# Kernel optimization log

Hardware: AMD Instinct MI355X
Metric: run time of the kernel (lower is better)

Reference implementation:

```python
import jax, jax.numpy as jnp
import numpy as np

EPS = 1e-5  # torch LayerNorm default
B, P, E, H = 16, 2048, 768, 256


def setup_inputs() -> dict:
    key = jax.random.key(0)
    k_x, k_qkv, k_lw = jax.random.split(key, 3)
    return {
        "x": jax.random.normal(k_x, (B, P, E), dtype=jnp.float32),
        "norm_w": jnp.ones((P, E), dtype=jnp.float32),
        "norm_b": jnp.zeros((P, E), dtype=jnp.float32),
        "qkv_w": jax.random.normal(k_qkv, (E, 3 * H), dtype=jnp.float32) * 0.02,
        "lin_w": jax.random.normal(k_lw, (E, H), dtype=jnp.float32) * 0.02,
        "lin_b": jnp.zeros((E,), dtype=jnp.float32),
    }


def reference(x, norm_w, norm_b, qkv_w, lin_w, lin_b):
    # LayerNorm over the last TWO dims (P, E) jointly, per batch element
    mean = jnp.mean(x, axis=(1, 2), keepdims=True)
    var = jnp.var(x, axis=(1, 2), keepdims=True)
    xn = (x - mean) * jax.lax.rsqrt(var + EPS) * norm_w + norm_b

    # QKV projection: [B,P,E] @ [E,3H] -> [B,P,3H]
    qkv = jnp.einsum("bpe,eh->bph", xn, qkv_w)
    q, k, v = jnp.split(qkv, 3, axis=2)  # each [B,P,H]

    # Unnormalized attention (no scale, no softmax)
    atten = jnp.einsum("bpd,bqd->bpq", q, k)  # [B,P,P]
    o = jnp.einsum("bpq,bqd->bpd", atten, v)  # [B,P,H]

    # Dropout p=0.0 (eval) -> identity; then Linear(H -> E) + ReLU
    out = jnp.einsum("bph,eh->bpe", o, lin_w) + lin_b
    return jax.nn.relu(out)
```

## Files before the change

kernel.cpp:

```cpp
#include <hip/hip_runtime.h>
#include <cstdio>
#include <cstdint>

typedef unsigned short u16;
typedef __bf16 bf16x8 __attribute__((ext_vector_type(8)));
typedef float floatx4 __attribute__((ext_vector_type(4)));

#define BB 16
#define PP 2048
#define EE 768
#define HH 256
#define PE (PP * EE)
#define MM (BB * PP)

__device__ __forceinline__ u16 f2bf(float f) {
  union { float f; uint32_t u; } v; v.f = f;
  return (u16)((v.u + 0x7fffu + ((v.u >> 16) & 1u)) >> 16);
}

__device__ __forceinline__ void gload16(const void* g, void* l) {
  typedef __attribute__((address_space(1))) const void GV;
  typedef __attribute__((address_space(3))) void LV;
  __builtin_amdgcn_global_load_lds((GV*)g, (LV*)l, 16, 0, 0);
}

__device__ __forceinline__ void zero_acc(floatx4 acc[4][4]) {
  const floatx4 z = {0.f, 0.f, 0.f, 0.f};
#pragma unroll
  for (int i = 0; i < 4; ++i)
#pragma unroll
    for (int j = 0; j < 4; ++j) acc[i][j] = z;
}

__device__ __forceinline__ void gemm_core(const u16* A, int lda, const u16* B, int ldb,
                                          int kIters, u16* As, u16* Bs,
                                          floatx4 acc[4][4]) {
  const int tid  = threadIdx.x;
  const int lane = tid & 63;
  const int wr   = (tid >> 7) & 1;
  const int wc   = (tid >> 6) & 1;
  const int srow = tid >> 3;
  const int scol = (tid & 7) << 3;
  const int mrow = lane & 15;
  const int kgrp = (lane >> 4) << 3;
  for (int kk = 0; kk < kIters; ++kk) {
    const u16* Ak = A + kk * 64;
    const u16* Bk = B + kk * 64;
    __syncthreads();
#pragma unroll
    for (int r = 0; r < 4; ++r) {
      gload16(Ak + (size_t)(r * 32 + srow) * lda + scol, (char*)As + r * 4096 + tid * 16);
      gload16(Bk + (size_t)(r * 32 + srow) * ldb + scol, (char*)Bs + r * 4096 + tid * 16);
    }
    __syncthreads();
#pragma unroll
    for (int kp = 0; kp < 2; ++kp) {
      const int ko = kp * 32 + kgrp;
      bf16x8 af[4], bq[4];
#pragma unroll
      for (int i = 0; i < 4; ++i) {
        af[i] = *(const bf16x8*)(As + (wr * 64 + i * 16 + mrow) * 64 + ko);
        bq[i] = *(const bf16x8*)(Bs + (wc * 64 + i * 16 + mrow) * 64 + ko);
      }
#pragma unroll
      for (int i = 0; i < 4; ++i)
#pragma unroll
        for (int j = 0; j < 4; ++j)
          acc[i][j] = __builtin_amdgcn_mfma_f32_16x16x32_bf16(af[i], bq[j], acc[i][j], 0, 0, 0);
    }
  }
}

template <typename F>
__device__ __forceinline__ void epilogue(floatx4 acc[4][4], F f) {
  const int lane = threadIdx.x & 63;
  const int wr = (threadIdx.x >> 7) & 1, wc = (threadIdx.x >> 6) & 1;
  const int r0 = (lane >> 4) * 4, c0 = lane & 15;
#pragma unroll
  for (int i = 0; i < 4; ++i)
#pragma unroll
    for (int j = 0; j < 4; ++j)
#pragma unroll
      for (int r = 0; r < 4; ++r)
        f(wr * 64 + i * 16 + r0 + r, wc * 64 + j * 16 + c0, acc[i][j][r]);
}

__global__ __launch_bounds__(256) void k_reduce1(const float* __restrict__ x,
                                                 float* __restrict__ psum,
                                                 float* __restrict__ psq) {
  const int b = blockIdx.y, blk = blockIdx.x, tid = threadIdx.x;
  const float4* xb = (const float4*)(x + (size_t)b * PE + (size_t)blk * 12288);
  float s = 0.f, q = 0.f;
#pragma unroll
  for (int i = 0; i < 12; ++i) {
    float4 v = xb[tid + i * 256];
    s += v.x + v.y + v.z + v.w;
    q += v.x * v.x + v.y * v.y + v.z * v.z + v.w * v.w;
  }
  for (int off = 32; off > 0; off >>= 1) { s += __shfl_down(s, off); q += __shfl_down(q, off); }
  __shared__ float ls[4], lq[4];
  if ((tid & 63) == 0) { ls[tid >> 6] = s; lq[tid >> 6] = q; }
  __syncthreads();
  if (tid == 0) {
    psum[b * 128 + blk] = ls[0] + ls[1] + ls[2] + ls[3];
    psq [b * 128 + blk] = lq[0] + lq[1] + lq[2] + lq[3];
  }
}

__global__ void k_reduce2(const float* __restrict__ psum, const float* __restrict__ psq,
                          float* __restrict__ stats) {
  const int b = blockIdx.x, tid = threadIdx.x;
  float s = psum[b * 128 + tid], q = psq[b * 128 + tid];
  for (int off = 32; off > 0; off >>= 1) { s += __shfl_down(s, off); q += __shfl_down(q, off); }
  __shared__ float ls[2], lq[2];
  if ((tid & 63) == 0) { ls[tid >> 6] = s; lq[tid >> 6] = q; }
  __syncthreads();
  if (tid == 0) {
    float S = ls[0] + ls[1], Q = lq[0] + lq[1];
    const float invN = 1.f / (float)PE;
    float mean = S * invN;
    float var = Q * invN - mean * mean;
    stats[b * 2] = mean;
    stats[b * 2 + 1] = rsqrtf(var + 1e-5f);
  }
}

__global__ __launch_bounds__(256) void k_ln(const float* __restrict__ x,
                                            const float* __restrict__ w,
                                            const float* __restrict__ bia,
                                            const float* __restrict__ stats,
                                            u16* __restrict__ xn) {
  const float4* x4 = (const float4*)x;
  const float4* w4 = (const float4*)w;
  const float4* b4 = (const float4*)bia;
  for (int vi = blockIdx.x * 256 + threadIdx.x; vi < (PE / 4) * BB; vi += gridDim.x * 256) {
    int bidx = vi / (PE / 4);
    int wi = vi - bidx * (PE / 4);
    float4 xv = x4[vi], wv = w4[wi], bv = b4[wi];
    float mean = stats[bidx * 2], rstd = stats[bidx * 2 + 1];
    ushort4 o;
    o.x = f2bf((xv.x - mean) * rstd * wv.x + bv.x);
    o.y = f2bf((xv.y - mean) * rstd * wv.y + bv.y);
    o.z = f2bf((xv.z - mean) * rstd * wv.z + bv.z);
    o.w = f2bf((xv.w - mean) * rstd * wv.w + bv.w);
    ((ushort4*)xn)[vi] = o;
  }
}

__global__ void k_transpose_w(const float* __restrict__ src, u16* __restrict__ dst) {
  __shared__ float t[32][33];
  const int e0 = blockIdx.x * 32, n0 = blockIdx.y * 32;
  const int tx = threadIdx.x, ty = threadIdx.y;
#pragma unroll
  for (int j = 0; j < 4; ++j)
    t[ty + j * 8][tx] = src[(size_t)(e0 + ty + j * 8) * 768 + n0 + tx];
  __syncthreads();
#pragma unroll
  for (int j = 0; j < 4; ++j)
    dst[(size_t)(n0 + ty + j * 8) * 768 + e0 + tx] = f2bf(t[tx][ty + j * 8]);
}

__global__ void k_cast(const float* __restrict__ src, u16* __restrict__ dst, int n4) {
  int i = blockIdx.x * 256 + threadIdx.x;
  if (i < n4) {
    float4 v = ((const float4*)src)[i];
    ushort4 o;
    o.x = f2bf(v.x); o.y = f2bf(v.y); o.z = f2bf(v.z); o.w = f2bf(v.w);
    ((ushort4*)dst)[i] = o;
  }
}

__global__ __launch_bounds__(256) void k_gemm_qkv(const u16* __restrict__ xn,
                                                  const u16* __restrict__ wT,
                                                  u16* __restrict__ qkv) {
  __shared__ __align__(16) u16 As[128 * 64], Bs[128 * 64];
  floatx4 acc[4][4];
  zero_acc(acc);
  const int tM = blockIdx.y * 128, tN = blockIdx.x * 128;
  gemm_core(xn + (size_t)tM * EE, EE, wT + (size_t)tN * EE, EE, 12, As, Bs, acc);
  epilogue(acc, [&](int gr, int gc, float v) {
    qkv[(size_t)(tM + gr) * EE + tN + gc] = f2bf(v);
  });
}

__global__ void k_transpose_kv(const u16* __restrict__ qkv, u16* __restrict__ kT,
                               u16* __restrict__ vT) {
  __shared__ u16 t[32][33];
  const int z = blockIdx.z, b = z >> 1, which = z & 1;
  const int p0 = blockIdx.x * 32, d0 = blockIdx.y * 32;
  const u16* src = qkv + (size_t)b * PE + HH + which * HH;
  u16* dst = (which ? vT : kT) + (size_t)b * (HH * PP);
  const int tx = threadIdx.x, ty = threadIdx.y;
#pragma unroll
  for (int j = 0; j < 4; ++j)
    t[ty + j * 8][tx] = src[(size_t)(p0 + ty + j * 8) * EE + d0 + tx];
  __syncthreads();
#pragma unroll
  for (int j = 0; j < 4; ++j)
    dst[(size_t)(d0 + ty + j * 8) * PP + p0 + tx] = t[tx][ty + j * 8];
}

__global__ __launch_bounds__(256) void k_gemm_wt(const u16* __restrict__ vT,
                                                 const u16* __restrict__ kT,
                                                 float* __restrict__ part) {
  __shared__ __align__(16) u16 As[128 * 64], Bs[128 * 64];
  floatx4 acc[4][4];
  zero_acc(acc);
  const int z = blockIdx.z, b = z >> 3, s = z & 7;
  const int tM = blockIdx.y * 128, tN = blockIdx.x * 128;
  const u16* A = vT + (size_t)b * (HH * PP) + (size_t)tM * PP + s * 256;
  const u16* B = kT + (size_t)b * (HH * PP) + (size_t)tN * PP + s * 256;
  gemm_core(A, PP, B, PP, 4, As, Bs, acc);
  float* P = part + (size_t)z * 65536;
  epilogue(acc, [&](int gr, int gc, float v) {
    P[(size_t)(tM + gr) * 256 + tN + gc] = v;
  });
}

__global__ void k_reduce_wt(const float* __restrict__ part, u16* __restrict__ Wt) {
  const int idx = blockIdx.x * 256 + threadIdx.x;
  const int b = idx >> 16, i = idx & 65535;
  const float* p = part + ((size_t)b << 19) + i;
  float s = 0.f;
#pragma unroll
  for (int t = 0; t < 8; ++t) s += p[(size_t)t << 16];
  Wt[idx] = f2bf(s);
}

__global__ __launch_bounds__(256) void k_gemm_o(const u16* __restrict__ qkv,
                                                const u16* __restrict__ Wt,
                                                u16* __restrict__ o) {
  __shared__ __align__(16) u16 As[128 * 64], Bs[128 * 64];
  floatx4 acc[4][4];
  zero_acc(acc);
  const int b = blockIdx.z;
  const int tM = blockIdx.y * 128, tN = blockIdx.x * 128;
  const u16* A = qkv + (size_t)b * PE + (size_t)tM * EE;
  const u16* B = Wt + (size_t)b * 65536 + (size_t)tN * 256;
  gemm_core(A, EE, B, 256, 4, As, Bs, acc);
  u16* ob = o + (size_t)b * (PP * HH);
  epilogue(acc, [&](int gr, int gc, float v) {
    ob[(size_t)(tM + gr) * HH + tN + gc] = f2bf(v);
  });
}

__global__ __launch_bounds__(256) void k_gemm_lin(const u16* __restrict__ o,
                                                  const u16* __restrict__ lw,
                                                  const float* __restrict__ lb,
                                                  float* __restrict__ out) {
  __shared__ __align__(16) u16 As[128 * 64], Bs[128 * 64];
  floatx4 acc[4][4];
  zero_acc(acc);
  const int tM = blockIdx.y * 128, tN = blockIdx.x * 128;
  gemm_core(o + (size_t)tM * HH, HH, lw + (size_t)tN * HH, HH, 4, As, Bs, acc);
  epilogue(acc, [&](int gr, int gc, float v) {
    out[(size_t)(tM + gr) * EE + tN + gc] = fmaxf(v + lb[tN + gc], 0.f);
  });
}

extern "C" void kernel_launch(void* const* d_in, const int* in_sizes, int n_in,
                              void* d_out, int out_size, void* d_ws, size_t ws_size,
                              hipStream_t stream) {
  (void)in_sizes; (void)n_in; (void)out_size;
  const float* x  = (const float*)d_in[0];
  const float* nw = (const float*)d_in[1];
  const float* nb = (const float*)d_in[2];
  const float* qw = (const float*)d_in[3];
  const float* lw = (const float*)d_in[4];
  const float* lb = (const float*)d_in[5];
  float* out = (float*)d_out;
  char* ws = (char*)d_ws;

  size_t off = 0;
  auto alloc = [&](size_t bytes) { size_t o = off; off += (bytes + 255) & ~(size_t)255; return o; };
  const size_t o_psum = alloc(16 * 128 * 4);
  const size_t o_psq  = alloc(16 * 128 * 4);
  const size_t o_st   = alloc(16 * 2 * 4);
  const size_t o_qwT  = alloc((size_t)768 * 768 * 2);
  const size_t o_lwB  = alloc((size_t)768 * 256 * 2);
  const size_t o_qkv  = alloc((size_t)MM * EE * 2);
  const size_t o_kT   = alloc((size_t)BB * HH * PP * 2);
  const size_t o_vT   = alloc((size_t)BB * HH * PP * 2);
  const size_t o_Wt   = alloc((size_t)BB * HH * HH * 2);
  const size_t need_base = off;
  const size_t region = (size_t)MM * EE * 2;

  char* big = (ws_size >= need_base + region) ? (ws + need_base) : (char*)d_out;
  static bool printed = false;
  if (!printed) {
    fprintf(stderr, "[vit] ws_size=%zu need=%zu big_in_out=%d\n",
            ws_size, need_base + region, big == (char*)d_out);
    printed = true;
  }

  float* psum = (float*)(ws + o_psum);
  float* psq  = (float*)(ws + o_psq);
  float* st   = (float*)(ws + o_st);
  u16* qwT    = (u16*)(ws + o_qwT);
  u16* lwB    = (u16*)(ws + o_lwB);
  u16* qkv    = (u16*)(ws + o_qkv);
  u16* kT     = (u16*)(ws + o_kT);
  u16* vT     = (u16*)(ws + o_vT);
  u16* Wt     = (u16*)(ws + o_Wt);
  u16* o_buf  = (u16*)(ws + o_kT);
  u16* xn     = (u16*)big;
  float* part = (float*)big;

  k_reduce1<<<dim3(128, 16), 256, 0, stream>>>(x, psum, psq);
  k_reduce2<<<16, 128, 0, stream>>>(psum, psq, st);
  k_ln<<<2048, 256, 0, stream>>>(x, nw, nb, st, xn);
  k_transpose_w<<<dim3(24, 24), dim3(32, 8), 0, stream>>>(qw, qwT);
  k_cast<<<192, 256, 0, stream>>>(lw, lwB, 768 * 256 / 4);
  k_gemm_qkv<<<dim3(6, 256), 256, 0, stream>>>(xn, qwT, qkv);
  k_transpose_kv<<<dim3(64, 8, 32), dim3(32, 8), 0, stream>>>(qkv, kT, vT);
  k_gemm_wt<<<dim3(2, 2, 128), 256, 0, stream>>>(vT, kT, part);
  k_reduce_wt<<<4096, 256, 0, stream>>>(part, Wt);
  k_gemm_o<<<dim3(2, 16, 16), 256, 0, stream>>>(qkv, Wt, o_buf);
  k_gemm_lin<<<dim3(6, 256), 256, 0, stream>>>(o_buf, lwB, lb, out);
}
```

Baseline: 354.6 us.

## Fold linear weight into per-batch KV product and fuse K/V transpose into QKV GEMM

Reassociates the chain so the per-batch K^T V matrix is multiplied by the linear weight first, giving a small per-batch 768x256 matrix. The output then comes from a single GEMM of Q against that matrix, removing the separate O GEMM and its intermediate buffer. The QKV GEMM epilogue now writes K and V already transposed through shared memory, which eliminates the standalone transpose kernel. All GEMMs use 1D grids with an XCD-aware block remap for cache locality. The extra bf16 rounding of the fused matrix can change numerical error slightly.

New measurement: 329.7 us. 1.08x faster.

```diff
diff --git a/kernel.cpp b/kernel.cpp
--- a/kernel.cpp
+++ b/kernel.cpp
@@ -1,5 +1,4 @@
 #include <hip/hip_runtime.h>
-#include <cstdio>
 #include <cstdint>
 
 typedef unsigned short u16;
@@ -22,6 +21,10 @@
   typedef __attribute__((address_space(1))) const void GV;
   typedef __attribute__((address_space(3))) void LV;
   __builtin_amdgcn_global_load_lds((GV*)g, (LV*)l, 16, 0, 0);
+}
+
+__device__ __forceinline__ int xcd_remap(int orig, int nwg) {
+  return (orig & 7) * (nwg >> 3) + (orig >> 3);
 }
 
 __device__ __forceinline__ void zero_acc(floatx4 acc[4][4]) {
@@ -172,44 +175,70 @@
 
 __global__ __launch_bounds__(256) void k_gemm_qkv(const u16* __restrict__ xn,
                                                   const u16* __restrict__ wT,
-                                                  u16* __restrict__ qkv) {
-  __shared__ __align__(16) u16 As[128 * 64], Bs[128 * 64];
+                                                  u16* __restrict__ q_buf,
+                                                  u16* __restrict__ kT,
+                                                  u16* __restrict__ vT) {
+  __shared__ __align__(16) u16 sbuf[128 * 64 * 2];
+  u16* As = sbuf;
+  u16* Bs = sbuf + 128 * 64;
   floatx4 acc[4][4];
   zero_acc(acc);
-  const int tM = blockIdx.y * 128, tN = blockIdx.x * 128;
+  const int t = xcd_remap(blockIdx.x, 1536);
+  const int xt = t % 6, yt = t / 6;
+  const int tM = yt * 128, tN = xt * 128;
   gemm_core(xn + (size_t)tM * EE, EE, wT + (size_t)tN * EE, EE, 12, As, Bs, acc);
-  epilogue(acc, [&](int gr, int gc, float v) {
-    qkv[(size_t)(tM + gr) * EE + tN + gc] = f2bf(v);
-  });
-}
-
-__global__ void k_transpose_kv(const u16* __restrict__ qkv, u16* __restrict__ kT,
-                               u16* __restrict__ vT) {
-  __shared__ u16 t[32][33];
-  const int z = blockIdx.z, b = z >> 1, which = z & 1;
-  const int p0 = blockIdx.x * 32, d0 = blockIdx.y * 32;
-  const u16* src = qkv + (size_t)b * PE + HH + which * HH;
-  u16* dst = (which ? vT : kT) + (size_t)b * (HH * PP);
-  const int tx = threadIdx.x, ty = threadIdx.y;
-#pragma unroll
-  for (int j = 0; j < 4; ++j)
-    t[ty + j * 8][tx] = src[(size_t)(p0 + ty + j * 8) * EE + d0 + tx];
-  __syncthreads();
-#pragma unroll
-  for (int j = 0; j < 4; ++j)
-    dst[(size_t)(d0 + ty + j * 8) * PP + p0 + tx] = t[tx][ty + j * 8];
-}
-
-__global__ __launch_bounds__(256) void k_gemm_wt(const u16* __restrict__ vT,
-                                                 const u16* __restrict__ kT,
+
+  if (xt < 2) {
+    epilogue(acc, [&](int gr, int gc, float v) {
+      q_buf[(size_t)(tM + gr) * HH + xt * 128 + gc] = f2bf(v);
+    });
+  } else {
+    const int b = yt >> 4;
+    const int p_base = (yt & 15) * 128;
+    u16* dst = ((xt < 4) ? kT : vT) + (size_t)b * (HH * PP);
+    const int dbase = (xt - ((xt < 4) ? 2 : 4)) * 128;
+    u16 (*tt)[144] = (u16(*)[144])sbuf;
+    const int tid = threadIdx.x;
+    const int lane = tid & 63;
+    const int wr = (tid >> 7) & 1, wc = (tid >> 6) & 1;
+    const int r0 = (lane >> 4) * 4, c0 = lane & 15;
+#pragma unroll
+    for (int h = 0; h < 2; ++h) {
+      __syncthreads();
+      if (wc == h) {
+#pragma unroll
+        for (int i = 0; i < 4; ++i)
+#pragma unroll
+          for (int j = 0; j < 4; ++j)
+#pragma unroll
+            for (int r = 0; r < 4; ++r)
+              tt[j * 16 + c0][wr * 64 + i * 16 + r0 + r] = f2bf(acc[i][j][r]);
+      }
+      __syncthreads();
+#pragma unroll
+      for (int pass = 0; pass < 4; ++pass) {
+        const int row = pass * 16 + (tid >> 4);
+        const int p8 = (tid & 15) * 8;
+        const int d = dbase + h * 64 + row;
+        uint4 vdat = *(const uint4*)&tt[row][p8];
+        *(uint4*)&dst[(size_t)d * PP + p_base + p8] = vdat;
+      }
+    }
+  }
+}
+
+__global__ __launch_bounds__(256) void k_gemm_w2(const u16* __restrict__ kT,
+                                                 const u16* __restrict__ vT,
                                                  float* __restrict__ part) {
   __shared__ __align__(16) u16 As[128 * 64], Bs[128 * 64];
   floatx4 acc[4][4];
   zero_acc(acc);
-  const int z = blockIdx.z, b = z >> 3, s = z & 7;
-  const int tM = blockIdx.y * 128, tN = blockIdx.x * 128;
-  const u16* A = vT + (size_t)b * (HH * PP) + (size_t)tM * PP + s * 256;
-  const u16* B = kT + (size_t)b * (HH * PP) + (size_t)tN * PP + s * 256;
+  const int t = xcd_remap(blockIdx.x, 512);
+  const int xt = t & 1, yt = (t >> 1) & 1, z = t >> 2;
+  const int b = z >> 3, s = z & 7;
+  const int tM = yt * 128, tN = xt * 128;
+  const u16* A = kT + (size_t)b * (HH * PP) + (size_t)tM * PP + s * 256;
+  const u16* B = vT + (size_t)b * (HH * PP) + (size_t)tN * PP + s * 256;
   gemm_core(A, PP, B, PP, 4, As, Bs, acc);
   float* P = part + (size_t)z * 65536;
   epilogue(acc, [&](int gr, int gc, float v) {
@@ -217,44 +246,50 @@
   });
 }
 
-__global__ void k_reduce_wt(const float* __restrict__ part, u16* __restrict__ Wt) {
+__global__ void k_reduce_w2(const float* __restrict__ part, u16* __restrict__ W2) {
   const int idx = blockIdx.x * 256 + threadIdx.x;
   const int b = idx >> 16, i = idx & 65535;
   const float* p = part + ((size_t)b << 19) + i;
   float s = 0.f;
 #pragma unroll
   for (int t = 0; t < 8; ++t) s += p[(size_t)t << 16];
-  Wt[idx] = f2bf(s);
-}
-
-__global__ __launch_bounds__(256) void k_gemm_o(const u16* __restrict__ qkv,
-                                                const u16* __restrict__ Wt,
-                                                u16* __restrict__ o) {
+  W2[idx] = f2bf(s);
+}
+
+__global__ __launch_bounds__(256) void k_gemm_m2(const u16* __restrict__ lwB,
+                                                 const u16* __restrict__ W2,
+                                                 u16* __restrict__ M2T) {
   __shared__ __align__(16) u16 As[128 * 64], Bs[128 * 64];
   floatx4 acc[4][4];
   zero_acc(acc);
-  const int b = blockIdx.z;
-  const int tM = blockIdx.y * 128, tN = blockIdx.x * 128;
-  const u16* A = qkv + (size_t)b * PE + (size_t)tM * EE;
-  const u16* B = Wt + (size_t)b * 65536 + (size_t)tN * 256;
-  gemm_core(A, EE, B, 256, 4, As, Bs, acc);
-  u16* ob = o + (size_t)b * (PP * HH);
+  const int t = xcd_remap(blockIdx.x, 192);
+  const int xt = t & 1, yt = (t >> 1) % 6, b = t / 12;
+  const int tM = yt * 128, tN = xt * 128;
+  const u16* A = lwB + (size_t)tM * HH;
+  const u16* B = W2 + (size_t)b * 65536 + (size_t)tN * HH;
+  gemm_core(A, HH, B, HH, 4, As, Bs, acc);
+  u16* Mb = M2T + (size_t)b * (EE * HH);
   epilogue(acc, [&](int gr, int gc, float v) {
-    ob[(size_t)(tM + gr) * HH + tN + gc] = f2bf(v);
+    Mb[(size_t)(tM + gr) * HH + tN + gc] = f2bf(v);
   });
 }
 
-__global__ __launch_bounds__(256) void k_gemm_lin(const u16* __restrict__ o,
-                                                  const u16* __restrict__ lw,
+__global__ __launch_bounds__(256) void k_gemm_out(const u16* __restrict__ q_buf,
+                                                  const u16* __restrict__ M2T,
                                                   const float* __restrict__ lb,
                                                   float* __restrict__ out) {
   __shared__ __align__(16) u16 As[128 * 64], Bs[128 * 64];
   floatx4 acc[4][4];
   zero_acc(acc);
-  const int tM = blockIdx.y * 128, tN = blockIdx.x * 128;
-  gemm_core(o + (size_t)tM * HH, HH, lw + (size_t)tN * HH, HH, 4, As, Bs, acc);
+  const int t = xcd_remap(blockIdx.x, 1536);
+  const int xt = t % 6, yt = (t / 6) % 16, b = t / 96;
+  const int tM = yt * 128, tN = xt * 128;
+  const u16* A = q_buf + (size_t)b * (PP * HH) + (size_t)tM * HH;
+  const u16* B = M2T + (size_t)b * (EE * HH) + (size_t)tN * HH;
+  gemm_core(A, HH, B, HH, 4, As, Bs, acc);
+  float* ob = out + (size_t)b * PE;
   epilogue(acc, [&](int gr, int gc, float v) {
-    out[(size_t)(tM + gr) * EE + tN + gc] = fmaxf(v + lb[tN + gc], 0.f);
+    ob[(size_t)(tM + gr) * EE + tN + gc] = fmaxf(v + lb[tN + gc], 0.f);
   });
 }
 
@@ -278,31 +313,26 @@
   const size_t o_st   = alloc(16 * 2 * 4);
   const size_t o_qwT  = alloc((size_t)768 * 768 * 2);
   const size_t o_lwB  = alloc((size_t)768 * 256 * 2);
-  const size_t o_qkv  = alloc((size_t)MM * EE * 2);
+  const size_t o_q    = alloc((size_t)MM * HH * 2);
   const size_t o_kT   = alloc((size_t)BB * HH * PP * 2);
   const size_t o_vT   = alloc((size_t)BB * HH * PP * 2);
-  const size_t o_Wt   = alloc((size_t)BB * HH * HH * 2);
+  const size_t o_W2   = alloc((size_t)BB * HH * HH * 2);
+  const size_t o_M2T  = alloc((size_t)BB * EE * HH * 2);
   const size_t need_base = off;
   const size_t region = (size_t)MM * EE * 2;
 
   char* big = (ws_size >= need_base + region) ? (ws + need_base) : (char*)d_out;
-  static bool printed = false;
-  if (!printed) {
-    fprintf(stderr, "[vit] ws_size=%zu need=%zu big_in_out=%d\n",
-            ws_size, need_base + region, big == (char*)d_out);
-    printed = true;
-  }
 
   float* psum = (float*)(ws + o_psum);
   float* psq  = (float*)(ws + o_psq);
   float* st   = (float*)(ws + o_st);
   u16* qwT    = (u16*)(ws + o_qwT);
   u16* lwB    = (u16*)(ws + o_lwB);
-  u16* qkv    = (u16*)(ws + o_qkv);
+  u16* q_buf  = (u16*)(ws + o_q);
   u16* kT     = (u16*)(ws + o_kT);
   u16* vT     = (u16*)(ws + o_vT);
-  u16* Wt     = (u16*)(ws + o_Wt);
-  u16* o_buf  = (u16*)(ws + o_kT);
+  u16* W2     = (u16*)(ws + o_W2);
+  u16* M2T    = (u16*)(ws + o_M2T);
   u16* xn     = (u16*)big;
   float* part = (float*)big;
 
@@ -311,10 +341,9 @@
   k_ln<<<2048, 256, 0, stream>>>(x, nw, nb, st, xn);
   k_transpose_w<<<dim3(24, 24), dim3(32, 8), 0, stream>>>(qw, qwT);
   k_cast<<<192, 256, 0, stream>>>(lw, lwB, 768 * 256 / 4);
-  k_gemm_qkv<<<dim3(6, 256), 256, 0, stream>>>(xn, qwT, qkv);
-  k_transpose_kv<<<dim3(64, 8, 32), dim3(32, 8), 0, stream>>>(qkv, kT, vT);
-  k_gemm_wt<<<dim3(2, 2, 128), 256, 0, stream>>>(vT, kT, part);
-  k_reduce_wt<<<4096, 256, 0, stream>>>(part, Wt);
-  k_gemm_o<<<dim3(2, 16, 16), 256, 0, stream>>>(qkv, Wt, o_buf);
-  k_gemm_lin<<<dim3(6, 256), 256, 0, stream>>>(o_buf, lwB, lb, out);
-}
+  k_gemm_qkv<<<1536, 256, 0, stream>>>(xn, qwT, q_buf, kT, vT);
+  k_gemm_w2<<<512, 256, 0, stream>>>(kT, vT, part);
+  k_reduce_w2<<<4096, 256, 0, stream>>>(part, W2);
+  k_gemm_m2<<<192, 256, 0, stream>>>(lwB, W2, M2T);
+  k_gemm_out<<<1536, 256, 0, stream>>>(q_buf, M2T, lb, out);
+}
```
